# Performance work log

Measured on AMD Instinct MI355X. Metric: run time of the kernel, lower is better.

Reference implementation:

```python
import jax, jax.numpy as jnp
import numpy as np

N_EMBD = 1024
N_HEAD = 16
BLOCK_SIZE = 2048
B, T = 4, 2048


def setup_inputs() -> dict:
    key = jax.random.key(0)
    ks = jax.random.split(key, 5)
    x = jax.random.normal(ks[0], (B, T, N_EMBD), dtype=jnp.float32)
    s_in = 1.0 / np.sqrt(N_EMBD)
    W_attn = jax.random.normal(ks[1], (N_EMBD, 3 * N_EMBD), dtype=jnp.float32) * s_in
    b_attn = jnp.zeros((3 * N_EMBD,), dtype=jnp.float32)
    W_proj = jax.random.normal(ks[2], (N_EMBD, N_EMBD), dtype=jnp.float32) * s_in
    b_proj = jnp.zeros((N_EMBD,), dtype=jnp.float32)
    return {"x": x, "W_attn": W_attn, "b_attn": b_attn, "W_proj": W_proj, "b_proj": b_proj}


def reference(x, W_attn, b_attn, W_proj, b_proj):
    Bb, Tt, C = x.shape
    hd = C // N_HEAD  # head_dim = 64
    qkv = x @ W_attn + b_attn                       # [B,T,3C]
    q, k, v = jnp.split(qkv, 3, axis=-1)
    q = q.reshape(Bb, Tt, N_HEAD, hd).transpose(0, 2, 1, 3)  # [B,H,T,hd]
    k = k.reshape(Bb, Tt, N_HEAD, hd).transpose(0, 2, 1, 3)
    v = v.reshape(Bb, Tt, N_HEAD, hd).transpose(0, 2, 1, 3)
    scores = jnp.einsum('bhqd,bhkd->bhqk', q, k) / jnp.sqrt(jnp.float32(hd))
    causal = jnp.tril(jnp.ones((Tt, Tt), dtype=bool))[None, None]
    scores = jnp.where(causal, scores, -jnp.inf)
    attn = jax.nn.softmax(scores, axis=-1)          # [B,H,T,T]
    y = jnp.einsum('bhqk,bhkd->bhqd', attn, v)      # [B,H,T,hd]
    y = y.transpose(0, 2, 1, 3).reshape(Bb, Tt, C)
    return y @ W_proj + b_proj
```

## Files before the change

kernel.cpp:

```cpp
#include <hip/hip_runtime.h>

#define N_EMBD 1024
#define N_HEAD 16
#define HD 64
#define BSZ 4
#define TSEQ 2048
#define MROWS (BSZ * TSEQ)

using bf16x8 = __attribute__((ext_vector_type(8))) short;
using f32x4  = __attribute__((ext_vector_type(4))) float;

__device__ __forceinline__ ushort f2bf(float f) {
    uint u = __float_as_uint(f);
    u += 0x7FFFu + ((u >> 16) & 1u);
    return (ushort)(u >> 16);
}
__device__ __forceinline__ float bf2f(ushort h) {
    return __uint_as_float(((uint)h) << 16);
}

__device__ __forceinline__ void gload16(const ushort* g, short* l) {
    __builtin_amdgcn_global_load_lds(
        (const __attribute__((address_space(1))) void*)g,
        (__attribute__((address_space(3))) void*)l, 16, 0, 0);
}

__global__ __launch_bounds__(256) void split_bf16(const float* __restrict__ A,
                                                  ushort* __restrict__ H,
                                                  ushort* __restrict__ L)
{
    const size_t i = ((size_t)blockIdx.x * 256 + threadIdx.x) * 4;
    const float4 v = *(const float4*)&A[i];
    ushort4 h, l;
    h.x = f2bf(v.x); l.x = f2bf(v.x - bf2f(h.x));
    h.y = f2bf(v.y); l.y = f2bf(v.y - bf2f(h.y));
    h.z = f2bf(v.z); l.z = f2bf(v.z - bf2f(h.z));
    h.w = f2bf(v.w); l.w = f2bf(v.w - bf2f(h.w));
    *(ushort4*)&H[i] = h;
    *(ushort4*)&L[i] = l;
}

__global__ __launch_bounds__(256) void transpose_split(
    const float* __restrict__ W, ushort* __restrict__ Th, ushort* __restrict__ Tl,
    int K, int N)
{
    __shared__ float t[32][33];
    const int k0 = blockIdx.y * 32;
    const int n0 = blockIdx.x * 32;
    const int c = threadIdx.x & 31;
    const int r = threadIdx.x >> 5;
    #pragma unroll
    for (int i = 0; i < 4; ++i)
        t[r + i * 8][c] = W[(size_t)(k0 + r + i * 8) * N + n0 + c];
    __syncthreads();
    #pragma unroll
    for (int i = 0; i < 4; ++i) {
        const float v = t[c][r + i * 8];
        const ushort hb = f2bf(v);
        const ushort lb = f2bf(v - bf2f(hb));
        const size_t o = (size_t)(n0 + r + i * 8) * K + k0 + c;
        Th[o] = hb;
        Tl[o] = lb;
    }
}

__global__ __launch_bounds__(256) void transpose_v(
    const ushort* __restrict__ qkvh, ushort* __restrict__ vth)
{
    __shared__ __align__(16) ushort tr[64][72];
    const int t0 = blockIdx.x * 64;
    const int h  = blockIdx.y;
    const int b  = blockIdx.z;
    const int r  = threadIdx.x >> 2;
    const int c4 = (threadIdx.x & 3) * 16;

    const size_t inb = ((size_t)(b * TSEQ + t0 + r)) * (3 * N_EMBD) + 2 * N_EMBD + h * HD + c4;
    *(float4*)&tr[r][c4]     = *(const float4*)&qkvh[inb];
    *(float4*)&tr[r][c4 + 8] = *(const float4*)&qkvh[inb + 8];
    __syncthreads();

    ushort v[16] __attribute__((aligned(16)));
    #pragma unroll
    for (int u = 0; u < 16; ++u) v[u] = tr[c4 + u][r];
    const size_t ob = (((size_t)(b * N_HEAD + h)) * HD + r) * TSEQ + t0 + c4;
    *(float4*)&vth[ob]     = ((const float4*)v)[0];
    *(float4*)&vth[ob + 8] = ((const float4*)v)[1];
}

template<bool ASPLIT, bool OUTBF16>
__global__ __launch_bounds__(256) void gemm_mfma(
    const ushort* __restrict__ Ah, const ushort* __restrict__ Al,
    const ushort* __restrict__ Bh, const ushort* __restrict__ Bl,
    const float* __restrict__ bias,
    float* __restrict__ Cf, ushort* __restrict__ Ch, ushort* __restrict__ Cl,
    int M, int N, int K)
{
    __shared__ __align__(16) short lds_raw[16384];

    const int tid  = threadIdx.x;
    const int wave = tid >> 6;
    const int lane = tid & 63;
    const int wr   = wave >> 1;
    const int wc   = wave & 1;
    const int row0 = blockIdx.y * 128;
    const int col0 = blockIdx.x * 128;

    const int sr  = wave * 32 + (lane >> 2);
    const int sco = (lane & 3) * 8;
    const ushort* gAh = Ah + (size_t)(row0 + sr) * K + sco;
    const ushort* gAl = ASPLIT ? (Al + (size_t)(row0 + sr) * K + sco) : nullptr;
    const ushort* gBh = Bh + (size_t)(col0 + sr) * K + sco;
    const ushort* gBl = Bl + (size_t)(col0 + sr) * K + sco;
    short* const ldst = lds_raw + wave * 1024;

    const int fr = lane & 15;
    const int fq = lane >> 4;
    const int ko = fq * 8;

    f32x4 acc[4][4] = {};

    for (int k0 = 0; k0 < K; k0 += 32) {
        const size_t K16 = (size_t)16 * K;
        gload16(gAh + k0,       ldst);
        gload16(gAh + k0 + K16, ldst + 512);
        if (ASPLIT) {
            gload16(gAl + k0,       ldst + 4096);
            gload16(gAl + k0 + K16, ldst + 4096 + 512);
        }
        gload16(gBh + k0,       ldst + 8192);
        gload16(gBh + k0 + K16, ldst + 8192 + 512);
        gload16(gBl + k0,       ldst + 12288);
        gload16(gBl + k0 + K16, ldst + 12288 + 512);
        __syncthreads();

        bf16x8 a_h[4], a_l[4], b_h[4], b_l[4];
        #pragma unroll
        for (int m = 0; m < 4; ++m) {
            const int r = wr * 64 + m * 16 + fr;
            a_h[m] = *(const bf16x8*)&lds_raw[r * 32 + ko];
            if (ASPLIT) a_l[m] = *(const bf16x8*)&lds_raw[4096 + r * 32 + ko];
        }
        #pragma unroll
        for (int n = 0; n < 4; ++n) {
            const int r = wc * 64 + n * 16 + fr;
            b_h[n] = *(const bf16x8*)&lds_raw[8192 + r * 32 + ko];
            b_l[n] = *(const bf16x8*)&lds_raw[12288 + r * 32 + ko];
        }

        #pragma unroll
        for (int m = 0; m < 4; ++m)
            #pragma unroll
            for (int n = 0; n < 4; ++n) {
                acc[m][n] = __builtin_amdgcn_mfma_f32_16x16x32_bf16(a_h[m], b_h[n], acc[m][n], 0, 0, 0);
                if (ASPLIT)
                    acc[m][n] = __builtin_amdgcn_mfma_f32_16x16x32_bf16(a_l[m], b_h[n], acc[m][n], 0, 0, 0);
                acc[m][n] = __builtin_amdgcn_mfma_f32_16x16x32_bf16(a_h[m], b_l[n], acc[m][n], 0, 0, 0);
            }
        __syncthreads();
    }

    float bv[4];
    #pragma unroll
    for (int n = 0; n < 4; ++n) bv[n] = bias[col0 + wc * 64 + n * 16 + fr];

    if (OUTBF16) {
        short* wbuf = lds_raw + wave * 2048;
        #pragma unroll
        for (int t = 0; t < 2; ++t) {
            ushort* dst = (t == 0) ? Ch : Cl;
            #pragma unroll
            for (int half = 0; half < 2; ++half) {
                __syncthreads();
                #pragma unroll
                for (int m2 = 0; m2 < 2; ++m2) {
                    const int m = half * 2 + m2;
                    #pragma unroll
                    for (int j = 0; j < 4; ++j)
                        #pragma unroll
                        for (int n = 0; n < 4; ++n) {
                            const float o = acc[m][n][j] + bv[n];
                            const ushort hb = f2bf(o);
                            wbuf[(m2 * 16 + fq * 4 + j) * 64 + n * 16 + fr] =
                                (short)(t == 0 ? hb : f2bf(o - bf2f(hb)));
                        }
                }
                __syncthreads();
                #pragma unroll
                for (int i = 0; i < 4; ++i) {
                    const int r = i * 8 + (lane >> 3);
                    const bf16x8 v = *(const bf16x8*)&wbuf[r * 64 + (lane & 7) * 8];
                    *(bf16x8*)&dst[(size_t)(row0 + wr * 64 + half * 32 + r) * N
                                   + col0 + wc * 64 + (lane & 7) * 8] = v;
                }
            }
        }
    } else {
        float* fbuf = (float*)lds_raw + wave * 2048;
        #pragma unroll
        for (int half = 0; half < 2; ++half) {
            __syncthreads();
            #pragma unroll
            for (int m2 = 0; m2 < 2; ++m2) {
                const int m = half * 2 + m2;
                #pragma unroll
                for (int j = 0; j < 4; ++j)
                    #pragma unroll
                    for (int n = 0; n < 4; ++n)
                        fbuf[(m2 * 16 + fq * 4 + j) * 64 + n * 16 + fr] = acc[m][n][j] + bv[n];
            }
            __syncthreads();
            #pragma unroll
            for (int i = 0; i < 8; ++i) {
                const int r = i * 4 + (lane >> 4);
                const float4 v = *(const float4*)&fbuf[r * 64 + (lane & 15) * 4];
                *(float4*)&Cf[(size_t)(row0 + wr * 64 + half * 32 + r) * N
                              + col0 + wc * 64 + (lane & 15) * 4] = v;
            }
        }
    }
}

__global__ __launch_bounds__(512, 4) void flash_attn_mfma(
    const ushort* __restrict__ qkvh, const ushort* __restrict__ qkvl,
    const ushort* __restrict__ vth, ushort* __restrict__ ath)
{
    __shared__ __align__(16) short Kh[64][72];
    __shared__ __align__(16) short Kl[64][72];
    __shared__ __align__(16) short Vs[64][72];
    __shared__ __align__(16) short Pw[8][2][16][72];

    const int tid  = threadIdx.x;
    const int wave = tid >> 6;
    const int lane = tid & 63;
    const int fr = lane & 15;
    const int g  = lane >> 4;
    const int q0 = blockIdx.x * 128;
    const int h  = blockIdx.y;
    const int b  = blockIdx.z;
    const int qw = q0 + wave * 16;
    const int qg = qw + fr;

    const size_t qrow = ((size_t)(b * TSEQ + qg)) * (3 * N_EMBD) + h * HD + 8 * g;
    const bf16x8 qh0 = *(const bf16x8*)&qkvh[qrow];
    const bf16x8 qh1 = *(const bf16x8*)&qkvh[qrow + 32];
    const bf16x8 ql0 = *(const bf16x8*)&qkvl[qrow];
    const bf16x8 ql1 = *(const bf16x8*)&qkvl[qrow + 32];

    f32x4 O[4] = {};
    float mrun = -1e30f, lrun = 0.f;

    const int sr = tid >> 3;
    const int sc = (tid & 7) * 8;
    const ushort* kgh = qkvh + ((size_t)(b * TSEQ + sr)) * (3 * N_EMBD) + N_EMBD + h * HD + sc;
    const ushort* kgl = qkvl + ((size_t)(b * TSEQ + sr)) * (3 * N_EMBD) + N_EMBD + h * HD + sc;
    const ushort* vg  = vth + (((size_t)(b * N_HEAD + h)) * HD + sr) * TSEQ + sc;

    const int nt = q0 / 64 + 2;
    for (int kt = 0; kt < nt; ++kt) {
        const float4 rkh = *(const float4*)(kgh + (size_t)kt * 64 * 3 * N_EMBD);
        const float4 rkl = *(const float4*)(kgl + (size_t)kt * 64 * 3 * N_EMBD);
        const float4 rv  = *(const float4*)(vg + kt * 64);
        __syncthreads();
        *(float4*)&Kh[sr][sc] = rkh;
        *(float4*)&Kl[sr][sc] = rkl;
        *(float4*)&Vs[sr][sc] = rv;
        __syncthreads();

        if (kt * 64 > qw + 15) continue;

        f32x4 s[4] = {};
        #pragma unroll
        for (int kf = 0; kf < 4; ++kf) {
            const bf16x8 kh0 = *(const bf16x8*)&Kh[kf * 16 + fr][8 * g];
            const bf16x8 kl0 = *(const bf16x8*)&Kl[kf * 16 + fr][8 * g];
            const bf16x8 kh1 = *(const bf16x8*)&Kh[kf * 16 + fr][32 + 8 * g];
            const bf16x8 kl1 = *(const bf16x8*)&Kl[kf * 16 + fr][32 + 8 * g];
            s[kf] = __builtin_amdgcn_mfma_f32_16x16x32_bf16(kh0, qh0, s[kf], 0, 0, 0);
            s[kf] = __builtin_amdgcn_mfma_f32_16x16x32_bf16(kl0, qh0, s[kf], 0, 0, 0);
            s[kf] = __builtin_amdgcn_mfma_f32_16x16x32_bf16(kh0, ql0, s[kf], 0, 0, 0);
            s[kf] = __builtin_amdgcn_mfma_f32_16x16x32_bf16(kh1, qh1, s[kf], 0, 0, 0);
            s[kf] = __builtin_amdgcn_mfma_f32_16x16x32_bf16(kl1, qh1, s[kf], 0, 0, 0);
            s[kf] = __builtin_amdgcn_mfma_f32_16x16x32_bf16(kh1, ql1, s[kf], 0, 0, 0);
        }

        const bool dm = (kt * 64 + 63 > qw);
        float tmax = -1e30f;
        #pragma unroll
        for (int kf = 0; kf < 4; ++kf)
            #pragma unroll
            for (int j = 0; j < 4; ++j) {
                float v = s[kf][j] * 0.125f;
                if (dm && (kt * 64 + kf * 16 + 4 * g + j > qg)) v = -1e30f;
                s[kf][j] = v;
                tmax = fmaxf(tmax, v);
            }
        tmax = fmaxf(tmax, __shfl_xor(tmax, 16));
        tmax = fmaxf(tmax, __shfl_xor(tmax, 32));
        const float mn = fmaxf(mrun, tmax);
        const float sf = __expf(mrun - mn);
        mrun = mn;
        lrun *= sf;
        #pragma unroll
        for (int df = 0; df < 4; ++df)
            #pragma unroll
            for (int j = 0; j < 4; ++j) O[df][j] *= sf;

        #pragma unroll
        for (int kf = 0; kf < 4; ++kf) {
            uint hw0, hw1, lw0, lw1;
            {
                const float p0 = __expf(s[kf][0] - mn);
                const float p1 = __expf(s[kf][1] - mn);
                const float p2 = __expf(s[kf][2] - mn);
                const float p3 = __expf(s[kf][3] - mn);
                const ushort h0 = f2bf(p0), h1 = f2bf(p1), h2 = f2bf(p2), h3 = f2bf(p3);
                const ushort l0 = f2bf(p0 - bf2f(h0)), l1 = f2bf(p1 - bf2f(h1));
                const ushort l2 = f2bf(p2 - bf2f(h2)), l3 = f2bf(p3 - bf2f(h3));
                lrun += (bf2f(h0) + bf2f(l0)) + (bf2f(h1) + bf2f(l1))
                      + (bf2f(h2) + bf2f(l2)) + (bf2f(h3) + bf2f(l3));
                hw0 = (uint)h0 | ((uint)h1 << 16);
                hw1 = (uint)h2 | ((uint)h3 << 16);
                lw0 = (uint)l0 | ((uint)l1 << 16);
                lw1 = (uint)l2 | ((uint)l3 << 16);
            }
            const int kb = kf * 16 + 4 * g;
            *(uint*)&Pw[wave][0][fr][kb]     = hw0;
            *(uint*)&Pw[wave][0][fr][kb + 2] = hw1;
            *(uint*)&Pw[wave][1][fr][kb]     = lw0;
            *(uint*)&Pw[wave][1][fr][kb + 2] = lw1;
        }

        #pragma unroll
        for (int c = 0; c < 2; ++c) {
            const bf16x8 pbh = *(const bf16x8*)&Pw[wave][0][fr][c * 32 + 8 * g];
            const bf16x8 pbl = *(const bf16x8*)&Pw[wave][1][fr][c * 32 + 8 * g];
            #pragma unroll
            for (int df = 0; df < 4; ++df) {
                const bf16x8 va = *(const bf16x8*)&Vs[df * 16 + fr][c * 32 + 8 * g];
                O[df] = __builtin_amdgcn_mfma_f32_16x16x32_bf16(va, pbh, O[df], 0, 0, 0);
                O[df] = __builtin_amdgcn_mfma_f32_16x16x32_bf16(va, pbl, O[df], 0, 0, 0);
            }
        }
    }

    lrun += __shfl_xor(lrun, 16);
    lrun += __shfl_xor(lrun, 32);
    const float inv = 1.f / lrun;

    float* Ol = (float*)&Pw[wave][0][0][0];
    #pragma unroll
    for (int df = 0; df < 4; ++df)
        #pragma unroll
        for (int j = 0; j < 4; ++j)
            Ol[fr * 68 + df * 16 + 4 * g + j] = O[df][j] * inv;

    const int q2 = lane >> 2;
    const int dl = (lane & 3) * 4;
    const size_t orow = ((size_t)(b * TSEQ + q0 + wave * 16 + q2)) * N_EMBD + h * HD;
    #pragma unroll
    for (int i = 0; i < 4; ++i) {
        const float4 y = *(const float4*)&Ol[q2 * 68 + dl + 16 * i];
        ushort4 o4;
        o4.x = f2bf(y.x); o4.y = f2bf(y.y); o4.z = f2bf(y.z); o4.w = f2bf(y.w);
        *(ushort4*)&ath[orow + dl + 16 * i] = o4;
    }
}

extern "C" void kernel_launch(void* const* d_in, const int* in_sizes, int n_in,
                              void* d_out, int out_size, void* d_ws, size_t ws_size,
                              hipStream_t stream) {
    const float* x      = (const float*)d_in[0];
    const float* W_attn = (const float*)d_in[1];
    const float* b_attn = (const float*)d_in[2];
    const float* W_proj = (const float*)d_in[3];
    const float* b_proj = (const float*)d_in[4];
    float* out = (float*)d_out;
    (void)in_sizes; (void)n_in; (void)out_size; (void)ws_size;

    char* ws = (char*)d_ws;
    ushort* qkvh = (ushort*)ws; ws += (size_t)MROWS * 3 * N_EMBD * 2;
    ushort* qkvl = (ushort*)ws; ws += (size_t)MROWS * 3 * N_EMBD * 2;
    ushort* xh   = (ushort*)ws; ws += (size_t)MROWS * N_EMBD * 2;
    ushort* xl   = (ushort*)ws; ws += (size_t)MROWS * N_EMBD * 2;
    ushort* wah  = (ushort*)ws; ws += (size_t)3 * N_EMBD * N_EMBD * 2;
    ushort* wal  = (ushort*)ws; ws += (size_t)3 * N_EMBD * N_EMBD * 2;
    ushort* wph  = (ushort*)ws; ws += (size_t)N_EMBD * N_EMBD * 2;
    ushort* wpl  = (ushort*)ws; ws += (size_t)N_EMBD * N_EMBD * 2;
    ushort* vth  = (ushort*)ws; ws += (size_t)MROWS * N_EMBD * 2;
    ushort* ath  = (ushort*)ws;

    dim3 blk(256);

    split_bf16<<<dim3(MROWS * N_EMBD / 1024), blk, 0, stream>>>(x, xh, xl);
    transpose_split<<<dim3(3 * N_EMBD / 32, N_EMBD / 32), blk, 0, stream>>>(
        W_attn, wah, wal, N_EMBD, 3 * N_EMBD);
    transpose_split<<<dim3(N_EMBD / 32, N_EMBD / 32), blk, 0, stream>>>(
        W_proj, wph, wpl, N_EMBD, N_EMBD);

    gemm_mfma<true, true><<<dim3(3 * N_EMBD / 128, MROWS / 128), blk, 0, stream>>>(
        xh, xl, wah, wal, b_attn, nullptr, qkvh, qkvl, MROWS, 3 * N_EMBD, N_EMBD);

    transpose_v<<<dim3(TSEQ / 64, N_HEAD, BSZ), blk, 0, stream>>>(qkvh, vth);

    flash_attn_mfma<<<dim3(TSEQ / 128, N_HEAD, BSZ), dim3(512), 0, stream>>>(
        qkvh, qkvl, vth, ath);

    gemm_mfma<false, false><<<dim3(N_EMBD / 128, MROWS / 128), blk, 0, stream>>>(
        ath, nullptr, wph, wpl, b_proj, out, nullptr, nullptr, MROWS, N_EMBD, N_EMBD);
}
```

Before: 545.7 us.

## Prefetch next K/V tile into registers, XOR-swizzle LDS, and raise MFMA priority

Moves the global loads for the next K/V tile ahead of the current tile's compute, double-buffering through registers so load latency overlaps the MFMA work. Replaces the padded 72-wide LDS rows with 64-wide rows plus an XOR swizzle on the 16-byte column chunk, which reduces LDS footprint and is meant to avoid bank conflicts. Wraps the MFMA loops in s_setprio so waves issuing matrix ops are favoured by the scheduler. The prefetch adds register pressure under launch_bounds(512,4), which could cause spills or reduce occupancy.

Result: faster. 515.8 us (-5.5%).

```diff
diff --git a/kernel.cpp b/kernel.cpp
--- a/kernel.cpp
+++ b/kernel.cpp
@@ -224,9 +224,9 @@
     const ushort* __restrict__ qkvh, const ushort* __restrict__ qkvl,
     const ushort* __restrict__ vth, ushort* __restrict__ ath)
 {
-    __shared__ __align__(16) short Kh[64][72];
-    __shared__ __align__(16) short Kl[64][72];
-    __shared__ __align__(16) short Vs[64][72];
+    __shared__ __align__(16) short Kh[64][64];
+    __shared__ __align__(16) short Kl[64][64];
+    __shared__ __align__(16) short Vs[64][64];
     __shared__ __align__(16) short Pw[8][2][16][72];
 
     const int tid  = threadIdx.x;
@@ -249,32 +249,48 @@
     f32x4 O[4] = {};
     float mrun = -1e30f, lrun = 0.f;
 
-    const int sr = tid >> 3;
-    const int sc = (tid & 7) * 8;
+    const int sr  = tid >> 3;
+    const int su  = tid & 7;
+    const int spu = (su ^ (sr & 7)) * 8;
+    const int sc  = su * 8;
     const ushort* kgh = qkvh + ((size_t)(b * TSEQ + sr)) * (3 * N_EMBD) + N_EMBD + h * HD + sc;
     const ushort* kgl = qkvl + ((size_t)(b * TSEQ + sr)) * (3 * N_EMBD) + N_EMBD + h * HD + sc;
     const ushort* vg  = vth + (((size_t)(b * N_HEAD + h)) * HD + sr) * TSEQ + sc;
 
+    const int x7  = fr & 7;
+    const int ru0 = (g ^ x7) * 8;
+    const int ru1 = ((4 + g) ^ x7) * 8;
+
     const int nt = q0 / 64 + 2;
+
+    float4 nkh = *(const float4*)(kgh);
+    float4 nkl = *(const float4*)(kgl);
+    float4 nv  = *(const float4*)(vg);
+
     for (int kt = 0; kt < nt; ++kt) {
-        const float4 rkh = *(const float4*)(kgh + (size_t)kt * 64 * 3 * N_EMBD);
-        const float4 rkl = *(const float4*)(kgl + (size_t)kt * 64 * 3 * N_EMBD);
-        const float4 rv  = *(const float4*)(vg + kt * 64);
         __syncthreads();
-        *(float4*)&Kh[sr][sc] = rkh;
-        *(float4*)&Kl[sr][sc] = rkl;
-        *(float4*)&Vs[sr][sc] = rv;
+        *(float4*)&Kh[sr][spu] = nkh;
+        *(float4*)&Kl[sr][spu] = nkl;
+        *(float4*)&Vs[sr][spu] = nv;
         __syncthreads();
 
+        if (kt + 1 < nt) {
+            nkh = *(const float4*)(kgh + (size_t)(kt + 1) * 64 * 3 * N_EMBD);
+            nkl = *(const float4*)(kgl + (size_t)(kt + 1) * 64 * 3 * N_EMBD);
+            nv  = *(const float4*)(vg + (kt + 1) * 64);
+        }
+
         if (kt * 64 > qw + 15) continue;
 
         f32x4 s[4] = {};
+        __builtin_amdgcn_s_setprio(1);
         #pragma unroll
         for (int kf = 0; kf < 4; ++kf) {
-            const bf16x8 kh0 = *(const bf16x8*)&Kh[kf * 16 + fr][8 * g];
-            const bf16x8 kl0 = *(const bf16x8*)&Kl[kf * 16 + fr][8 * g];
-            const bf16x8 kh1 = *(const bf16x8*)&Kh[kf * 16 + fr][32 + 8 * g];
-            const bf16x8 kl1 = *(const bf16x8*)&Kl[kf * 16 + fr][32 + 8 * g];
+            const int kr = kf * 16 + fr;
+            const bf16x8 kh0 = *(const bf16x8*)&Kh[kr][ru0];
+            const bf16x8 kl0 = *(const bf16x8*)&Kl[kr][ru0];
+            const bf16x8 kh1 = *(const bf16x8*)&Kh[kr][ru1];
+            const bf16x8 kl1 = *(const bf16x8*)&Kl[kr][ru1];
             s[kf] = __builtin_amdgcn_mfma_f32_16x16x32_bf16(kh0, qh0, s[kf], 0, 0, 0);
             s[kf] = __builtin_amdgcn_mfma_f32_16x16x32_bf16(kl0, qh0, s[kf], 0, 0, 0);
             s[kf] = __builtin_amdgcn_mfma_f32_16x16x32_bf16(kh0, ql0, s[kf], 0, 0, 0);
@@ -282,6 +298,7 @@
             s[kf] = __builtin_amdgcn_mfma_f32_16x16x32_bf16(kl1, qh1, s[kf], 0, 0, 0);
             s[kf] = __builtin_amdgcn_mfma_f32_16x16x32_bf16(kh1, ql1, s[kf], 0, 0, 0);
         }
+        __builtin_amdgcn_s_setprio(0);
 
         const bool dm = (kt * 64 + 63 > qw);
         float tmax = -1e30f;
@@ -334,12 +351,15 @@
         for (int c = 0; c < 2; ++c) {
             const bf16x8 pbh = *(const bf16x8*)&Pw[wave][0][fr][c * 32 + 8 * g];
             const bf16x8 pbl = *(const bf16x8*)&Pw[wave][1][fr][c * 32 + 8 * g];
+            const int rvc = ((4 * c + g) ^ x7) * 8;
+            __builtin_amdgcn_s_setprio(1);
             #pragma unroll
             for (int df = 0; df < 4; ++df) {
-                const bf16x8 va = *(const bf16x8*)&Vs[df * 16 + fr][c * 32 + 8 * g];
+                const bf16x8 va = *(const bf16x8*)&Vs[df * 16 + fr][rvc];
                 O[df] = __builtin_amdgcn_mfma_f32_16x16x32_bf16(va, pbh, O[df], 0, 0, 0);
                 O[df] = __builtin_amdgcn_mfma_f32_16x16x32_bf16(va, pbl, O[df], 0, 0, 0);
             }
+            __builtin_amdgcn_s_setprio(0);
         }
     }
 
```
